# Optimization experiments

Measured on AMD Instinct MI355X. Metric: run time of the kernel, lower is better.

The kernel has to match this reference:

```python
import jax, jax.numpy as jnp
import numpy as np

N_STROKES = 512
H = 256
W = 256
EPS = 1e-6


def setup_inputs() -> dict:
    key = jax.random.key(0)
    k1, k2, k3, k4, k5, k6 = jax.random.split(key, 6)
    canvas = jnp.zeros((3, H, W), dtype=jnp.float32)
    target = jax.random.uniform(k1, (3, H, W), dtype=jnp.float32)
    offset = jax.random.normal(k2, (N_STROKES, 2, 1), dtype=jnp.float32) * 0.5 + 0.5
    sigma = jax.random.uniform(k3, (N_STROKES, 2, 1), dtype=jnp.float32) * 0.5 + 0.2
    theta = jax.random.uniform(k4, (N_STROKES, 1), dtype=jnp.float32) * (2.0 * np.pi)
    color = jax.random.uniform(k5, (N_STROKES, 3, 1, 1), dtype=jnp.float32)
    alpha = jax.random.normal(k6, (N_STROKES, 1, 1, 1), dtype=jnp.float32) * 0.1
    return {"canvas": canvas, "target": target, "offset": offset,
            "sigma": sigma, "theta": theta, "color": color, "alpha": alpha}


def reference(canvas, target, offset, sigma, theta, color, alpha):
    h, w = canvas.shape[-2:]
    ratio = w / h  # width_to_height_ratio

    # normalized pixel grid, matching torch.linspace(0, w-1, w)/w
    ws = jnp.arange(w, dtype=jnp.float32) / w
    hs = jnp.arange(h, dtype=jnp.float32) / h
    x, y = jnp.meshgrid(ws, hs, indexing="xy")          # (H, W) each
    coords = jnp.stack([x, y], axis=0).reshape(1, 2, -1)  # (1, 2, H*W)
    coords = coords - offset                              # (n, 2, H*W)

    # rotation matrix per stroke: [[cos, -sin], [sin, -cos]] (as in source)
    cos_t = jnp.cos(theta)
    sin_t = jnp.sin(theta)
    rot = jnp.concatenate([cos_t, -sin_t, sin_t, -cos_t], axis=-1).reshape(-1, 2, 2)
    coords = jnp.einsum("nij,njp->nip", rot, coords)      # (n, 2, H*W)

    # aspect-corrected sigma (only for the gaussian field, not the loss)
    sig = jnp.concatenate([sigma[:, :1] / ratio, sigma[:, 1:]], axis=1)  # (n, 2, 1)

    quad = jnp.sum(jnp.square(coords) / (2.0 * jnp.square(sig)), axis=1)  # (n, H*W)
    pdf = jnp.exp(-quad)
    maxes = jnp.max(pdf, axis=-1, keepdims=True)          # per-stroke max-normalize
    pdf = pdf / (maxes + EPS)

    strokes = pdf.reshape(-1, 1, h, w) * alpha * color    # (n, 3, H, W)
    out = jax.nn.sigmoid(canvas + jnp.sum(strokes, axis=0))

    # loss_fn(out, target)
    l2 = jnp.mean(jnp.square(out - target))
    sharpness = jnp.mean(jnp.abs(1.0 - sigma[:, 0] / sigma[:, 1])) * 0.001
    transparency = -jnp.mean(jnp.abs(alpha)) * 0.001
    mse = jnp.mean(jnp.square(target - out))
    psnr = 10.0 * jnp.log10(1.0 / (mse + 1e-12))
    loss = l2 + transparency + sharpness - psnr / 30.0
    return out, loss
```

## Files before the change

kernel.cpp:

```cpp
#include <hip/hip_runtime.h>
#include <hip/hip_bf16.h>

#define HH 256
#define WW 256
#define NPIX (HH*WW)
#define NS 512

#define A_P  0
#define A_Q  1
#define A_T1 2
#define A_R  3
#define A_S  4
#define A_T2 5
#define A_C0 6
#define A_C1 7
#define A_C2 8
#define A_SH 9
#define A_TR 10
#define L2_SLOT  (11*NS)
#define CNT_SLOT (11*NS + 1)

#define TEAMS 16
#define SPT   (NS/TEAMS)
#define PPT   4
#define BLK   1024
#define K2_GRID 256

#define L2E 1.4426950408889634f

#if __has_builtin(__builtin_amdgcn_exp2f)
#define EXP2F(x) __builtin_amdgcn_exp2f(x)
#else
#define EXP2F(x) exp2f(x)
#endif
#if __has_builtin(__builtin_amdgcn_rcpf)
#define RCPF(x) __builtin_amdgcn_rcpf(x)
#else
#define RCPF(x) (1.0f/(x))
#endif

__device__ __forceinline__ float rlane(float v, int l) {
#if __has_builtin(__builtin_amdgcn_readlane)
    return __int_as_float(__builtin_amdgcn_readlane(__float_as_int(v), l));
#else
    return __shfl(v, l, 64);
#endif
}

__global__ __launch_bounds__(256) void k1_prep(
    const float* __restrict__ offset, const float* __restrict__ sigma,
    const float* __restrict__ theta,  const float* __restrict__ color,
    const float* __restrict__ alpha,  float* __restrict__ wsf)
{
    const int n = blockIdx.x;
    const int i = threadIdx.x;

    const float ox = offset[2*n], oy = offset[2*n+1];
    const float s0 = sigma[2*n],  s1 = sigma[2*n+1];
    const float th = theta[n];

    const float kk = sqrtf(0.5f * L2E);
    const float ra = kk / s0;
    const float rb = kk / s1;

    float s, c;
    __sincosf(th, &s, &c);
    const float P = ra * c,  Q = -ra * s,  T1 = ra * (-c * ox + s * oy);
    const float R = rb * s,  S = -rb * c,  T2 = rb * (-s * ox + c * oy);

    const float y     = (float)i / (float)HH;
    const float beta  = fmaf(Q, y, T1);
    const float delta = fmaf(S, y, T2);
    const float A     = P * P + R * R;
    const float xstar = -(P * beta + R * delta) / A;
    int j0 = (int)floorf(xstar * (float)WW);
    j0 = max(0, min(WW - 1, j0));
    const int j1 = min(WW - 1, j0 + 1);
    const float x0 = (float)j0 / (float)WW, x1 = (float)j1 / (float)WW;
    const float u0 = fmaf(P, x0, beta),  v0 = fmaf(R, x0, delta);
    const float u1 = fmaf(P, x1, beta),  v1 = fmaf(R, x1, delta);
    float q = fminf(u0*u0 + v0*v0, u1*u1 + v1*v1);

    #pragma unroll
    for (int off = 32; off > 0; off >>= 1)
        q = fminf(q, __shfl_down(q, off));
    __shared__ float wmin[4];
    if ((i & 63) == 0) wmin[i >> 6] = q;
    __syncthreads();

    if (i == 0) {
        const float qmin   = fminf(fminf(wmin[0], wmin[1]), fminf(wmin[2], wmin[3]));
        const float maxpdf = EXP2F(-qmin);
        const float base   = alpha[n] / (maxpdf + 1e-6f);
        wsf[A_P *NS + n] = P;
        wsf[A_Q *NS + n] = Q;
        wsf[A_T1*NS + n] = T1;
        wsf[A_R *NS + n] = R;
        wsf[A_S *NS + n] = S;
        wsf[A_T2*NS + n] = T2;
        wsf[A_C0*NS + n] = base * color[3*n];
        wsf[A_C1*NS + n] = base * color[3*n+1];
        wsf[A_C2*NS + n] = base * color[3*n+2];
        wsf[A_SH*NS + n] = fabsf(1.0f - s0 / s1);
        wsf[A_TR*NS + n] = fabsf(alpha[n]);
        if (n == 0) {
            wsf[L2_SLOT] = 0.0f;
            ((int*)wsf)[CNT_SLOT] = 0;
        }
    }
}

__global__ __launch_bounds__(1024) void k2_paint(
    const float* __restrict__ canvas, const float* __restrict__ target,
    const float* __restrict__ prm,    float* __restrict__ out,
    float* __restrict__ l2acc,        int* __restrict__ cnt)
{
    const int tid  = threadIdx.x;
    const int t    = tid & 63;
    const int w    = tid >> 6;
    const int row  = blockIdx.x;
    const float y  = (float)row * (1.0f / (float)HH);

    float rP = 0.0f, rR = 0.0f, rB = 0.0f, rD = 0.0f;
    float rc0 = 0.0f, rc1 = 0.0f, rc2 = 0.0f;
    if (t < SPT) {
        const int n = w * SPT + t;
        rP  = prm[A_P *NS + n];
        rR  = prm[A_R *NS + n];
        rB  = fmaf(prm[A_Q*NS + n], y, prm[A_T1*NS + n]);
        rD  = fmaf(prm[A_S*NS + n], y, prm[A_T2*NS + n]);
        rc0 = prm[A_C0*NS + n];
        rc1 = prm[A_C1*NS + n];
        rc2 = prm[A_C2*NS + n];
    }

    float xk[PPT];
    #pragma unroll
    for (int k = 0; k < PPT; ++k) xk[k] = (float)(t + 64*k) * (1.0f / (float)WW);

    float acc[PPT][3] = {};
    #pragma unroll
    for (int n = 0; n < SPT; ++n) {
        const float P  = rlane(rP,  n);
        const float R  = rlane(rR,  n);
        const float B  = rlane(rB,  n);
        const float D  = rlane(rD,  n);
        const float c0 = rlane(rc0, n);
        const float c1 = rlane(rc1, n);
        const float c2 = rlane(rc2, n);
        #pragma unroll
        for (int k = 0; k < PPT; ++k) {
            const float U = fmaf(P, xk[k], B);
            const float V = fmaf(R, xk[k], D);
            const float e = EXP2F(-fmaf(U, U, V * V));
            acc[k][0] = fmaf(e, c0, acc[k][0]);
            acc[k][1] = fmaf(e, c1, acc[k][1]);
            acc[k][2] = fmaf(e, c2, acc[k][2]);
        }
    }

    __shared__ float sacc[TEAMS][WW][3];
    #pragma unroll
    for (int k = 0; k < PPT; ++k) {
        sacc[w][t + 64*k][0] = acc[k][0];
        sacc[w][t + 64*k][1] = acc[k][1];
        sacc[w][t + 64*k][2] = acc[k][2];
    }
    __syncthreads();

    __shared__ float lw[4];
    __shared__ int sdone;
    if (tid < WW) {
        float z0 = 0.0f, z1 = 0.0f, z2 = 0.0f;
        #pragma unroll
        for (int tm = 0; tm < TEAMS; ++tm) {
            z0 += sacc[tm][tid][0];
            z1 += sacc[tm][tid][1];
            z2 += sacc[tm][tid][2];
        }
        const int p = row * WW + tid;
        z0 += canvas[p];
        z1 += canvas[NPIX + p];
        z2 += canvas[2*NPIX + p];
        const float o0 = RCPF(1.0f + EXP2F(-z0 * L2E));
        const float o1 = RCPF(1.0f + EXP2F(-z1 * L2E));
        const float o2 = RCPF(1.0f + EXP2F(-z2 * L2E));
        out[p]          = o0;
        out[NPIX + p]   = o1;
        out[2*NPIX + p] = o2;
        const float d0 = o0 - target[p];
        const float d1 = o1 - target[NPIX + p];
        const float d2 = o2 - target[2*NPIX + p];
        float l2loc = d0*d0 + d1*d1 + d2*d2;
        #pragma unroll
        for (int off = 32; off > 0; off >>= 1)
            l2loc += __shfl_down(l2loc, off);
        if (t == 0) lw[tid >> 6] = l2loc;
    }
    __syncthreads();

    if (tid == 0) {
        atomicAdd(l2acc, lw[0] + lw[1] + lw[2] + lw[3]);
        __threadfence();
        const int old = atomicAdd(cnt, 1);
        sdone = (old == K2_GRID - 1) ? 1 : 0;
    }
    __syncthreads();

    if (sdone) {
        if (tid < NS) {
            float sh = prm[A_SH*NS + tid];
            float tr = prm[A_TR*NS + tid];
            #pragma unroll
            for (int off = 32; off > 0; off >>= 1) {
                sh += __shfl_down(sh, off);
                tr += __shfl_down(tr, off);
            }
            if (t == 0) { sacc[0][w][0] = sh; sacc[0][w][1] = tr; }
        }
        __syncthreads();
        if (tid == 0) {
            float shs = 0.0f, trs = 0.0f;
            #pragma unroll
            for (int v = 0; v < NS/64; ++v) { shs += sacc[0][v][0]; trs += sacc[0][v][1]; }
            const float l2tot  = atomicAdd(l2acc, 0.0f);
            const float l2     = l2tot / (float)(3 * NPIX);
            const float sharp  = (shs / (float)NS) * 0.001f;
            const float transp = -(trs / (float)NS) * 0.001f;
            const float psnr   = 10.0f * log10f(1.0f / (l2 + 1e-12f));
            out[3 * NPIX] = l2 + transp + sharp - psnr / 30.0f;
        }
    }
}

extern "C" void kernel_launch(void* const* d_in, const int* in_sizes, int n_in,
                              void* d_out, int out_size, void* d_ws, size_t ws_size,
                              hipStream_t stream)
{
    const float* canvas = (const float*)d_in[0];
    const float* target = (const float*)d_in[1];
    const float* offset = (const float*)d_in[2];
    const float* sigma  = (const float*)d_in[3];
    const float* theta  = (const float*)d_in[4];
    const float* color  = (const float*)d_in[5];
    const float* alpha  = (const float*)d_in[6];
    float* out = (float*)d_out;
    float* wsf = (float*)d_ws;

    k1_prep<<<NS, 256, 0, stream>>>(offset, sigma, theta, color, alpha, wsf);
    k2_paint<<<K2_GRID, BLK, 0, stream>>>(canvas, target, wsf, out,
                                          wsf + L2_SLOT, (int*)wsf + CNT_SLOT);
}
```

Measured before the change: 86.24 us.

## Collapse rotated Gaussian to per-row quadratic in x, halve team count

The prep kernel now expands the squared rotated coordinates into quadratic coefficients in x and y. The paint kernel evaluates the exponent with two FMAs per pixel instead of four ops, and broadcasts six values per stroke instead of seven. Teams drop from 16 to 8, so each wave walks 64 strokes and blocks are 512 threads, using every lane for the per-stroke loads. This raises per-wave loop length and register pressure, and the expanded polynomial may lose precision through cancellation for large coordinates.

```diff
diff --git a/kernel.cpp b/kernel.cpp
--- a/kernel.cpp
+++ b/kernel.cpp
@@ -6,24 +6,24 @@
 #define NPIX (HH*WW)
 #define NS 512
 
-#define A_P  0
-#define A_Q  1
-#define A_T1 2
-#define A_R  3
-#define A_S  4
-#define A_T2 5
-#define A_C0 6
-#define A_C1 7
-#define A_C2 8
-#define A_SH 9
-#define A_TR 10
+#define A_A2   0
+#define A_A1Y  1
+#define A_A1C  2
+#define A_A0YY 3
+#define A_A0Y  4
+#define A_A0C  5
+#define A_C0   6
+#define A_C1   7
+#define A_C2   8
+#define A_SH   9
+#define A_TR   10
 #define L2_SLOT  (11*NS)
 #define CNT_SLOT (11*NS + 1)
 
-#define TEAMS 16
+#define TEAMS 8
 #define SPT   (NS/TEAMS)
 #define PPT   4
-#define BLK   1024
+#define BLK   512
 #define K2_GRID 256
 
 #define L2E 1.4426950408889634f
@@ -92,17 +92,17 @@
         const float qmin   = fminf(fminf(wmin[0], wmin[1]), fminf(wmin[2], wmin[3]));
         const float maxpdf = EXP2F(-qmin);
         const float base   = alpha[n] / (maxpdf + 1e-6f);
-        wsf[A_P *NS + n] = P;
-        wsf[A_Q *NS + n] = Q;
-        wsf[A_T1*NS + n] = T1;
-        wsf[A_R *NS + n] = R;
-        wsf[A_S *NS + n] = S;
-        wsf[A_T2*NS + n] = T2;
-        wsf[A_C0*NS + n] = base * color[3*n];
-        wsf[A_C1*NS + n] = base * color[3*n+1];
-        wsf[A_C2*NS + n] = base * color[3*n+2];
-        wsf[A_SH*NS + n] = fabsf(1.0f - s0 / s1);
-        wsf[A_TR*NS + n] = fabsf(alpha[n]);
+        wsf[A_A2  *NS + n] = P * P + R * R;
+        wsf[A_A1Y *NS + n] = 2.0f * (P * Q + R * S);
+        wsf[A_A1C *NS + n] = 2.0f * (P * T1 + R * T2);
+        wsf[A_A0YY*NS + n] = Q * Q + S * S;
+        wsf[A_A0Y *NS + n] = 2.0f * (Q * T1 + S * T2);
+        wsf[A_A0C *NS + n] = T1 * T1 + T2 * T2;
+        wsf[A_C0  *NS + n] = base * color[3*n];
+        wsf[A_C1  *NS + n] = base * color[3*n+1];
+        wsf[A_C2  *NS + n] = base * color[3*n+2];
+        wsf[A_SH  *NS + n] = fabsf(1.0f - s0 / s1);
+        wsf[A_TR  *NS + n] = fabsf(alpha[n]);
         if (n == 0) {
             wsf[L2_SLOT] = 0.0f;
             ((int*)wsf)[CNT_SLOT] = 0;
@@ -110,7 +110,7 @@
     }
 }
 
-__global__ __launch_bounds__(1024) void k2_paint(
+__global__ __launch_bounds__(512) void k2_paint(
     const float* __restrict__ canvas, const float* __restrict__ target,
     const float* __restrict__ prm,    float* __restrict__ out,
     float* __restrict__ l2acc,        int* __restrict__ cnt)
@@ -121,14 +121,13 @@
     const int row  = blockIdx.x;
     const float y  = (float)row * (1.0f / (float)HH);
 
-    float rP = 0.0f, rR = 0.0f, rB = 0.0f, rD = 0.0f;
-    float rc0 = 0.0f, rc1 = 0.0f, rc2 = 0.0f;
-    if (t < SPT) {
+    float ra2, ra1, ra0, rc0, rc1, rc2;
+    {
         const int n = w * SPT + t;
-        rP  = prm[A_P *NS + n];
-        rR  = prm[A_R *NS + n];
-        rB  = fmaf(prm[A_Q*NS + n], y, prm[A_T1*NS + n]);
-        rD  = fmaf(prm[A_S*NS + n], y, prm[A_T2*NS + n]);
+        ra2 = prm[A_A2*NS + n];
+        ra1 = fmaf(prm[A_A1Y*NS + n], y, prm[A_A1C*NS + n]);
+        ra0 = fmaf(fmaf(prm[A_A0YY*NS + n], y, prm[A_A0Y*NS + n]), y,
+                   prm[A_A0C*NS + n]);
         rc0 = prm[A_C0*NS + n];
         rc1 = prm[A_C1*NS + n];
         rc2 = prm[A_C2*NS + n];
@@ -141,18 +140,17 @@
     float acc[PPT][3] = {};
     #pragma unroll
     for (int n = 0; n < SPT; ++n) {
-        const float P  = rlane(rP,  n);
-        const float R  = rlane(rR,  n);
-        const float B  = rlane(rB,  n);
-        const float D  = rlane(rD,  n);
+        const float a2 = rlane(ra2, n);
+        const float a1 = rlane(ra1, n);
+        const float a0 = rlane(ra0, n);
         const float c0 = rlane(rc0, n);
         const float c1 = rlane(rc1, n);
         const float c2 = rlane(rc2, n);
         #pragma unroll
         for (int k = 0; k < PPT; ++k) {
-            const float U = fmaf(P, xk[k], B);
-            const float V = fmaf(R, xk[k], D);
-            const float e = EXP2F(-fmaf(U, U, V * V));
+            const float tq = fmaf(a2, xk[k], a1);
+            const float q  = fmaf(tq, xk[k], a0);
+            const float e  = EXP2F(-q);
             acc[k][0] = fmaf(e, c0, acc[k][0]);
             acc[k][1] = fmaf(e, c1, acc[k][1]);
             acc[k][2] = fmaf(e, c2, acc[k][2]);
@@ -208,21 +206,19 @@
     __syncthreads();
 
     if (sdone) {
-        if (tid < NS) {
-            float sh = prm[A_SH*NS + tid];
-            float tr = prm[A_TR*NS + tid];
-            #pragma unroll
-            for (int off = 32; off > 0; off >>= 1) {
-                sh += __shfl_down(sh, off);
-                tr += __shfl_down(tr, off);
-            }
-            if (t == 0) { sacc[0][w][0] = sh; sacc[0][w][1] = tr; }
-        }
+        float sh = prm[A_SH*NS + tid];
+        float tr = prm[A_TR*NS + tid];
+        #pragma unroll
+        for (int off = 32; off > 0; off >>= 1) {
+            sh += __shfl_down(sh, off);
+            tr += __shfl_down(tr, off);
+        }
+        if (t == 0) { sacc[0][w][0] = sh; sacc[0][w][1] = tr; }
         __syncthreads();
         if (tid == 0) {
             float shs = 0.0f, trs = 0.0f;
             #pragma unroll
-            for (int v = 0; v < NS/64; ++v) { shs += sacc[0][v][0]; trs += sacc[0][v][1]; }
+            for (int v = 0; v < TEAMS; ++v) { shs += sacc[0][v][0]; trs += sacc[0][v][1]; }
             const float l2tot  = atomicAdd(l2acc, 0.0f);
             const float l2     = l2tot / (float)(3 * NPIX);
             const float sharp  = (shs / (float)NS) * 0.001f;
```

Measured after the change: 86.54 us. No clear change (+0.3%).
